# Optimization experiments

Hardware: AMD Instinct MI355X
Metric: run time of the kernel (lower is better)

Reference implementation:

```python
import jax, jax.numpy as jnp
import numpy as np

WS = 14            # window side (14x14 patches)
DIM = 768          # model dim (ViT-Base)
H = 12             # heads
HD = DIM // H      # head dim = 64
B = 128            # batch
N = WS * WS + 1    # 197 tokens (patches + CLS)
NRD = (2 * WS - 1) ** 2 + 3  # num_relative_distance = 732


def _rel_index():
    # Faithful replication of the torch buffer construction.
    coords = np.stack(np.meshgrid(np.arange(WS), np.arange(WS), indexing='ij'))  # [2,WS,WS]
    flat = coords.reshape(2, -1)                                   # [2, WS*WS]
    rel = flat[:, :, None] - flat[:, None, :]                      # [2, P, P]
    rel = rel.transpose(1, 2, 0).astype(np.int64)                  # [P, P, 2]
    rel[:, :, 0] += WS - 1
    rel[:, :, 1] += WS - 1
    rel[:, :, 0] *= 2 * WS - 1
    idx = np.zeros((N, N), dtype=np.int64)
    idx[1:, 1:] = rel.sum(-1)
    idx[0, :] = NRD - 3
    idx[:, 0] = NRD - 2
    idx[0, 0] = NRD - 1
    return jnp.asarray(idx, dtype=jnp.int32)


def setup_inputs() -> dict:
    key = jax.random.key(0)
    ks = jax.random.split(key, 5)
    return {
        'x': jax.random.normal(ks[0], (B, N, DIM), dtype=jnp.float32),
        'qkv_w': jax.random.normal(ks[1], (3 * DIM, DIM), dtype=jnp.float32) * 0.02,
        'q_bias': jnp.zeros((DIM,), jnp.float32),
        'v_bias': jnp.zeros((DIM,), jnp.float32),
        'rpb_table': jax.random.normal(ks[2], (NRD, H), dtype=jnp.float32) * 0.02,
        'proj_w': jax.random.normal(ks[3], (DIM, DIM), dtype=jnp.float32) * 0.02,
        'proj_b': jnp.zeros((DIM,), jnp.float32),
        'rel_idx': _rel_index(),
    }


def reference(x, qkv_w, q_bias, v_bias, rpb_table, proj_w, proj_b, rel_idx):
    Bv, Nv, C = x.shape
    scale = HD ** -0.5
    # qkv_bias = cat(q_bias, zeros, v_bias); eval mode so dropout is identity
    bias = jnp.concatenate([q_bias, jnp.zeros_like(v_bias), v_bias])
    qkv = x @ qkv_w.T + bias                                   # [B,N,3*DIM]
    qkv = qkv.reshape(Bv, Nv, 3, H, HD).transpose(2, 0, 3, 1, 4)
    q, k, v = qkv[0] * scale, qkv[1], qkv[2]                   # [B,H,N,HD]
    attn = jnp.einsum('bhqd,bhkd->bhqk', q, k)                 # [B,H,N,N]
    rpb = rpb_table[rel_idx]                                   # gather -> [N,N,H]
    attn = attn + rpb.transpose(2, 0, 1)[None]                 # + [1,H,N,N]
    attn = jax.nn.softmax(attn, axis=-1)
    out = jnp.einsum('bhqk,bhkd->bhqd', attn, v)               # [B,H,N,HD]
    out = out.transpose(0, 2, 1, 3).reshape(Bv, Nv, H * HD)
    return out @ proj_w.T + proj_b
```

## Files before the change

### kernel.cpp

```cpp
#include <hip/hip_runtime.h>
#include <hip/hip_bf16.h>
#include <cstdint>

#define BATCH 128
#define NTOK  197
#define NHEAD 12

typedef __attribute__((ext_vector_type(8))) __bf16 bf16x8;
typedef __attribute__((ext_vector_type(4))) float f32x4;
typedef __attribute__((ext_vector_type(4))) unsigned short ushort4v;

#define KSTR 72

__device__ __forceinline__ unsigned short f2bf(float f) {
    union { float f; unsigned int u; } v; v.f = f;
    unsigned int r = (v.u + 0x7FFFu + ((v.u >> 16) & 1u)) >> 16;
    return (unsigned short)r;
}

__device__ __forceinline__ void async_cp16(const void* gsrc, void* lds_dst) {
    __builtin_amdgcn_global_load_lds(
        (const __attribute__((address_space(1))) unsigned int*)((uintptr_t)gsrc),
        (__attribute__((address_space(3))) unsigned int*)((uintptr_t)lds_dst),
        16, 0, 0);
}

__global__ void bias_tiles(const float* __restrict__ rpb,
                           const int* __restrict__ rel_idx,
                           float* __restrict__ BT) {
    int idx = blockIdx.x * 256 + threadIdx.x;
    int r    = idx & 3;
    int j    = (idx >> 2) & 3;
    int l16  = (idx >> 4) & 15;
    int quad = (idx >> 8) & 3;
    int kt   = (idx >> 10) & 3;
    int qt   = (idx >> 12) & 15;
    int h    = idx >> 16;
    int qn = qt * 16 + quad * 4 + r; if (qn > 196) qn = 196;
    int kn = kt * 64 + j * 16 + l16;
    float v = 0.f;
    if (kn < NTOK) v = rpb[rel_idx[qn * NTOK + kn] * NHEAD + h];
    BT[idx] = v;
}

__global__ __launch_bounds__(256) void cvt_bf16(const float4* __restrict__ src,
                                                ushort4v* __restrict__ dst, int n4) {
    int i = blockIdx.x * 256 + threadIdx.x;
    if (i >= n4) return;
    float4 f = src[i];
    ushort4v o;
    o.x = f2bf(f.x); o.y = f2bf(f.y); o.z = f2bf(f.z); o.w = f2bf(f.w);
    dst[i] = o;
}

template <int EPI>
__global__ __launch_bounds__(512, 2) void gemm_mfma(
    const unsigned short* __restrict__ A,
    const unsigned short* __restrict__ W,
    const float* __restrict__ bias1, const float* __restrict__ bias2,
    unsigned short* __restrict__ oq, unsigned short* __restrict__ ok,
    unsigned short* __restrict__ ov, float* __restrict__ outf,
    int Mc) {
    __shared__ unsigned short lds[65536];

    const int t    = threadIdx.x;
    const int lane = t & 63;
    const int wave = t >> 6;
    const int wm   = wave >> 2;
    const int wn   = wave & 3;
    const int quad = lane >> 4;
    const int l16  = lane & 15;
    const int m0   = blockIdx.y * 256;
    const int n0   = blockIdx.x * 256;

    const int srow = wave * 8 + (lane >> 3);
    const int scol = (((lane & 7) ^ (lane >> 3)) << 3);
    const unsigned short* Asrc[4];
    const unsigned short* Wsrc[4];
#pragma unroll
    for (int l = 0; l < 4; l++) {
        int ra = m0 + l * 64 + srow; if (ra >= Mc) ra = Mc - 1;
        Asrc[l] = A + (size_t)ra * 768 + scol;
        Wsrc[l] = W + (size_t)(n0 + l * 64 + srow) * 768 + scol;
    }

    auto stage = [&](int c, int kt) {
        unsigned short* Ab = lds + c * 32768;
        unsigned short* Bb = Ab + 16384;
#pragma unroll
        for (int l = 0; l < 4; l++) {
            async_cp16(Asrc[l] + kt * 64, Ab + (l * 64 + wave * 8) * 64);
            async_cp16(Wsrc[l] + kt * 64, Bb + (l * 64 + wave * 8) * 64);
        }
    };

    const int arow0 = wm * 128 + l16;
    const int brow0 = wn * 64 + l16;
    const int csw0  = ((quad ^ (l16 & 7)) << 3);
    const int csw1  = (((4 + quad) ^ (l16 & 7)) << 3);

    f32x4 acc[8][4] = {};

    stage(0, 0);
#pragma unroll 1
    for (int kt = 0; kt < 12; kt++) {
        const int c = kt & 1;
        if (kt < 11) {
            stage(c ^ 1, kt + 1);
            asm volatile("s_waitcnt vmcnt(8)" ::: "memory");
        } else {
            asm volatile("s_waitcnt vmcnt(0)" ::: "memory");
        }
        __builtin_amdgcn_s_barrier();
        __builtin_amdgcn_sched_barrier(0);

        const unsigned short* Ab = lds + c * 32768;
        const unsigned short* Bb = Ab + 16384;

        bf16x8 bfr[4][2];
#pragma unroll
        for (int nf = 0; nf < 4; nf++) {
            bfr[nf][0] = *(const bf16x8*)(Bb + (brow0 + nf * 16) * 64 + csw0);
            bfr[nf][1] = *(const bf16x8*)(Bb + (brow0 + nf * 16) * 64 + csw1);
        }
#pragma unroll
        for (int p = 0; p < 4; p++) {
            bf16x8 af[2][2];
#pragma unroll
            for (int i = 0; i < 2; i++) {
                af[i][0] = *(const bf16x8*)(Ab + (arow0 + (p * 2 + i) * 16) * 64 + csw0);
                af[i][1] = *(const bf16x8*)(Ab + (arow0 + (p * 2 + i) * 16) * 64 + csw1);
            }
            __builtin_amdgcn_s_barrier();
            __builtin_amdgcn_sched_barrier(0);
            __builtin_amdgcn_s_setprio(1);
#pragma unroll
            for (int kk = 0; kk < 2; kk++)
#pragma unroll
                for (int i = 0; i < 2; i++)
#pragma unroll
                    for (int nf = 0; nf < 4; nf++)
                        acc[p * 2 + i][nf] = __builtin_amdgcn_mfma_f32_16x16x32_bf16(
                            af[i][kk], bfr[nf][kk], acc[p * 2 + i][nf], 0, 0, 0);
            __builtin_amdgcn_s_setprio(0);
            __builtin_amdgcn_sched_barrier(0);
            __builtin_amdgcn_s_barrier();
        }
    }

    if (EPI == 0) {
        const int part   = n0 / 768;
        const float scale = (part == 0) ? 0.125f : 1.f;
        unsigned short* dst = (part == 0) ? oq : (part == 1 ? ok : ov);
        const int nb = (n0 - part * 768) + wn * 64;
        const int h  = nb >> 6;
#pragma unroll
        for (int nf = 0; nf < 4; nf++) {
            const int d = nf * 16 + l16;
            const float bb = (part == 0) ? bias1[nb + nf * 16 + l16]
                           : (part == 2 ? bias2[nb + nf * 16 + l16] : 0.f);
#pragma unroll
            for (int mf = 0; mf < 8; mf++) {
                const int mb = m0 + wm * 128 + mf * 16 + quad * 4;
#pragma unroll
                for (int r = 0; r < 4; r++) {
                    const int m = mb + r;
                    if (m < Mc) {
                        const int bi  = m / NTOK;
                        const int tok = m - bi * NTOK;
                        dst[(((size_t)bi * NHEAD + h) * NTOK + tok) * 64 + d] =
                            f2bf((acc[mf][nf][r] + bb) * scale);
                    }
                }
            }
        }
    } else {
#pragma unroll
        for (int nf = 0; nf < 4; nf++) {
            const int col = n0 + wn * 64 + nf * 16 + l16;
            const float bb = bias1[col];
#pragma unroll
            for (int mf = 0; mf < 8; mf++) {
                const int mb = m0 + wm * 128 + mf * 16 + quad * 4;
#pragma unroll
                for (int r = 0; r < 4; r++) {
                    const int m = mb + r;
                    if (m < Mc) outf[(size_t)m * 768 + col] = acc[mf][nf][r] + bb;
                }
            }
        }
    }
}

__global__ __launch_bounds__(256, 2) void attn_mfma(
    const unsigned short* __restrict__ Q, const unsigned short* __restrict__ K,
    const unsigned short* __restrict__ V, const float* __restrict__ BT,
    unsigned short* __restrict__ AO) {
    __shared__ unsigned short Ks[64 * KSTR];
    __shared__ unsigned short Vt[64 * KSTR];
    __shared__ unsigned short Ps[4][64 * KSTR];

    const int t    = threadIdx.x;
    const int lane = t & 63;
    const int wave = t >> 6;
    const int quad = lane >> 4;
    const int l16  = lane & 15;
    const int bh   = blockIdx.x;
    const int b    = bh / NHEAD;
    const int h    = bh - b * NHEAD;

    const unsigned short* qb = Q + (size_t)bh * NTOK * 64;
    const unsigned short* kb = K + (size_t)bh * NTOK * 64;
    const unsigned short* vb = V + (size_t)bh * NTOK * 64;

    bf16x8 qf[4][2];
#pragma unroll
    for (int i = 0; i < 4; i++) {
        int tok = wave * 64 + i * 16 + l16; if (tok > 196) tok = 196;
#pragma unroll
        for (int ks = 0; ks < 2; ks++)
            qf[i][ks] = *(const bf16x8*)&qb[(size_t)tok * 64 + ks * 32 + quad * 8];
    }

    f32x4 O[4][4] = {};
    float lsum[4][4] = {};

    for (int kt = 0; kt < 4; kt++) {
        __syncthreads();
        {
            const int row = t >> 2, cg = t & 3;
            int gk = kt * 64 + row; if (gk > 196) gk = 196;
            const uint4* src = (const uint4*)&kb[(size_t)gk * 64 + cg * 16];
            *(uint4*)&Ks[row * KSTR + cg * 16]     = src[0];
            *(uint4*)&Ks[row * KSTR + cg * 16 + 8] = src[1];
        }
        {
            const int key = t & 63, dg = t >> 6;
            int gk = kt * 64 + key; if (gk > 196) gk = 196;
            union { uint4 v4[2]; unsigned short u[16]; } tmp;
            const uint4* src = (const uint4*)&vb[(size_t)gk * 64 + dg * 16];
            tmp.v4[0] = src[0]; tmp.v4[1] = src[1];
#pragma unroll
            for (int u = 0; u < 16; u++) Vt[(dg * 16 + u) * KSTR + key] = tmp.u[u];
        }
        __syncthreads();

        f32x4 acc[4][4];
#pragma unroll
        for (int i = 0; i < 4; i++) {
            const float4* bp = (const float4*)&BT[
                (((((size_t)h * 16 + (wave * 4 + i)) * 4 + kt) * 4 + quad) * 16 + l16) * 16];
#pragma unroll
            for (int j = 0; j < 4; j++) {
                float4 f = bp[j];
                acc[i][j] = (f32x4){f.x, f.y, f.z, f.w};
            }
        }

#pragma unroll
        for (int ks = 0; ks < 2; ks++) {
            bf16x8 kf[4];
#pragma unroll
            for (int j = 0; j < 4; j++)
                kf[j] = *(const bf16x8*)&Ks[(j * 16 + l16) * KSTR + ks * 32 + quad * 8];
#pragma unroll
            for (int i = 0; i < 4; i++)
#pragma unroll
                for (int j = 0; j < 4; j++)
                    acc[i][j] = __builtin_amdgcn_mfma_f32_16x16x32_bf16(
                        qf[i][ks], kf[j], acc[i][j], 0, 0, 0);
        }

#pragma unroll
        for (int j = 0; j < 4; j++) {
            const int kn = kt * 64 + j * 16 + l16;
            const bool kval = (kn < NTOK);
#pragma unroll
            for (int i = 0; i < 4; i++)
#pragma unroll
                for (int r = 0; r < 4; r++) {
                    float p = kval ? __expf(fminf(acc[i][j][r], 30.f)) : 0.f;
                    lsum[i][r] += p;
                    Ps[wave][(i * 16 + quad * 4 + r) * KSTR + j * 16 + l16] = f2bf(p);
                }
        }

#pragma unroll
        for (int ks = 0; ks < 2; ks++) {
            bf16x8 vf[4], pf[4];
#pragma unroll
            for (int jd = 0; jd < 4; jd++)
                vf[jd] = *(const bf16x8*)&Vt[(jd * 16 + l16) * KSTR + ks * 32 + quad * 8];
#pragma unroll
            for (int i = 0; i < 4; i++)
                pf[i] = *(const bf16x8*)&Ps[wave][(i * 16 + l16) * KSTR + ks * 32 + quad * 8];
#pragma unroll
            for (int i = 0; i < 4; i++)
#pragma unroll
                for (int jd = 0; jd < 4; jd++)
                    O[i][jd] = __builtin_amdgcn_mfma_f32_16x16x32_bf16(
                        pf[i], vf[jd], O[i][jd], 0, 0, 0);
        }
    }

#pragma unroll
    for (int i = 0; i < 4; i++)
#pragma unroll
        for (int r = 0; r < 4; r++) {
            float l = lsum[i][r];
            l += __shfl_xor(l, 1); l += __shfl_xor(l, 2);
            l += __shfl_xor(l, 4); l += __shfl_xor(l, 8);
            lsum[i][r] = 1.f / l;
        }
#pragma unroll
    for (int i = 0; i < 4; i++) {
        const int tb = wave * 64 + i * 16 + quad * 4;
#pragma unroll
        for (int r = 0; r < 4; r++) {
            const int tok = tb + r;
            if (tok < NTOK) {
                const float rl = lsum[i][r];
#pragma unroll
                for (int jd = 0; jd < 4; jd++)
                    AO[((size_t)b * NTOK + tok) * 768 + h * 64 + jd * 16 + l16] =
                        f2bf(O[i][jd][r] * rl);
            }
        }
    }
}

extern "C" void kernel_launch(void* const* d_in, const int* in_sizes, int n_in,
                              void* d_out, int out_size, void* d_ws, size_t ws_size,
                              hipStream_t stream) {
    const float* x      = (const float*)d_in[0];
    const float* qkv_w  = (const float*)d_in[1];
    const float* q_bias = (const float*)d_in[2];
    const float* v_bias = (const float*)d_in[3];
    const float* rpb    = (const float*)d_in[4];
    const float* proj_w = (const float*)d_in[5];
    const float* proj_b = (const float*)d_in[6];
    const int*   rel_idx = (const int*)d_in[7];
    float* out = (float*)d_out;

    const size_t EB   = 151296;
    const size_t NBT  = 786432;
    const size_t NX   = (size_t)BATCH * NTOK * 768;
    const size_t NWQ  = (size_t)2304 * 768;
    const size_t NWP  = (size_t)768 * 768;

    const size_t fixed_bytes = NBT * 4 + (NX + NWQ + NWP) * 2;
    int Bc = BATCH;
    while (Bc > 1 && fixed_bytes + 8ull * Bc * EB > ws_size) Bc >>= 1;
    if (fixed_bytes + 8ull * Bc * EB > ws_size) return;
    const int nc = BATCH / Bc;
    const int Mc = Bc * NTOK;
    const int Gy = (Mc + 255) / 256;

    float* BT             = (float*)d_ws;
    unsigned short* xbf   = (unsigned short*)(BT + NBT);
    unsigned short* wqkv  = xbf + NX;
    unsigned short* wproj = wqkv + NWQ;
    unsigned short* q     = wproj + NWP;
    unsigned short* k     = q + (size_t)Bc * EB;
    unsigned short* v     = k + (size_t)Bc * EB;
    unsigned short* aobf  = v + (size_t)Bc * EB;

    bias_tiles<<<(int)(NBT / 256), 256, 0, stream>>>(rpb, rel_idx, BT);
    cvt_bf16<<<(int)((NX / 4 + 255) / 256), 256, 0, stream>>>(
        (const float4*)x, (ushort4v*)xbf, (int)(NX / 4));
    cvt_bf16<<<(int)((NWQ / 4 + 255) / 256), 256, 0, stream>>>(
        (const float4*)qkv_w, (ushort4v*)wqkv, (int)(NWQ / 4));
    cvt_bf16<<<(int)((NWP / 4 + 255) / 256), 256, 0, stream>>>(
        (const float4*)proj_w, (ushort4v*)wproj, (int)(NWP / 4));

    for (int c = 0; c < nc; c++) {
        gemm_mfma<0><<<dim3(2304 / 256, Gy), 512, 0, stream>>>(
            xbf + (size_t)c * Mc * 768, wqkv, q_bias, v_bias, q, k, v, nullptr, Mc);
        attn_mfma<<<Bc * NHEAD, 256, 0, stream>>>(q, k, v, BT, aobf);
        gemm_mfma<1><<<dim3(768 / 256, Gy), 512, 0, stream>>>(
            aobf, wproj, proj_b, nullptr, nullptr, nullptr, nullptr,
            out + (size_t)c * Mc * 768, Mc);
    }
}
```

Measured before the change: 501.4 us.

## Remap workgroups per XCD and interleave half-tile prefetch with MFMA phases

Workgroup IDs are remapped so consecutive tiles land on the same XCD, aiming for better L2 reuse of A/W tiles. The global-to-LDS prefetch of the next K-tile is split into quarter stages issued inside the first two MFMA phases instead of all at once before compute. Per-phase trailing barriers are replaced by one waitcnt plus barrier per k-iteration. This targets load/compute overlap and barrier overhead, at the risk of LDS hazards if ordering is wrong.

```diff
diff --git a/kernel.cpp b/kernel.cpp
--- a/kernel.cpp
+++ b/kernel.cpp
@@ -70,68 +70,72 @@
     const int wn   = wave & 3;
     const int quad = lane >> 4;
     const int l16  = lane & 15;
-    const int m0   = blockIdx.y * 256;
-    const int n0   = blockIdx.x * 256;
+
+    const int gx  = gridDim.x;
+    const int nwg = gx * gridDim.y;
+    const int orig = blockIdx.y * gx + blockIdx.x;
+    const int q8 = nwg >> 3, r8 = nwg & 7;
+    const int xcd = orig & 7, rest = orig >> 3;
+    const int wg = (xcd < r8 ? xcd * (q8 + 1) : r8 * (q8 + 1) + (xcd - r8) * q8) + rest;
+    const int m0 = (wg / gx) * 256;
+    const int n0 = (wg % gx) * 256;
 
     const int srow = wave * 8 + (lane >> 3);
     const int scol = (((lane & 7) ^ (lane >> 3)) << 3);
-    const unsigned short* Asrc[4];
-    const unsigned short* Wsrc[4];
-#pragma unroll
-    for (int l = 0; l < 4; l++) {
-        int ra = m0 + l * 64 + srow; if (ra >= Mc) ra = Mc - 1;
-        Asrc[l] = A + (size_t)ra * 768 + scol;
-        Wsrc[l] = W + (size_t)(n0 + l * 64 + srow) * 768 + scol;
-    }
-
-    auto stage = [&](int c, int kt) {
-        unsigned short* Ab = lds + c * 32768;
-        unsigned short* Bb = Ab + 16384;
-#pragma unroll
-        for (int l = 0; l < 4; l++) {
-            async_cp16(Asrc[l] + kt * 64, Ab + (l * 64 + wave * 8) * 64);
-            async_cp16(Wsrc[l] + kt * 64, Bb + (l * 64 + wave * 8) * 64);
-        }
+    const unsigned short* gsrc[4][2];
+#pragma unroll
+    for (int hh = 0; hh < 2; hh++)
+#pragma unroll
+        for (int i = 0; i < 2; i++) {
+            int ra = m0 + hh * 128 + i * 64 + srow; if (ra >= Mc) ra = Mc - 1;
+            gsrc[hh][i]     = A + (size_t)ra * 768 + scol;
+            gsrc[2 + hh][i] = W + (size_t)(n0 + hh * 128 + i * 64 + srow) * 768 + scol;
+        }
+
+    auto stageHalf = [&](int b, int kt, int ht) {
+        unsigned short* dst = lds + b * 32768 + ht * 8192;
+        async_cp16(gsrc[ht][0] + kt * 64, dst + (wave * 8) * 64);
+        async_cp16(gsrc[ht][1] + kt * 64, dst + (64 + wave * 8) * 64);
     };
 
-    const int arow0 = wm * 128 + l16;
-    const int brow0 = wn * 64 + l16;
-    const int csw0  = ((quad ^ (l16 & 7)) << 3);
-    const int csw1  = (((4 + quad) ^ (l16 & 7)) << 3);
+    const int csw0 = ((quad ^ (l16 & 7)) << 3);
+    const int csw1 = (((4 + quad) ^ (l16 & 7)) << 3);
+    const int brow = (wn & 1) * 64 + l16;
 
     f32x4 acc[8][4] = {};
 
-    stage(0, 0);
-#pragma unroll 1
+#pragma unroll
+    for (int ht = 0; ht < 4; ht++) stageHalf(0, 0, ht);
+    asm volatile("s_waitcnt vmcnt(0)" ::: "memory");
+    __builtin_amdgcn_s_barrier();
+
+#pragma unroll 2
     for (int kt = 0; kt < 12; kt++) {
-        const int c = kt & 1;
-        if (kt < 11) {
-            stage(c ^ 1, kt + 1);
-            asm volatile("s_waitcnt vmcnt(8)" ::: "memory");
-        } else {
-            asm volatile("s_waitcnt vmcnt(0)" ::: "memory");
-        }
-        __builtin_amdgcn_s_barrier();
-        __builtin_amdgcn_sched_barrier(0);
-
-        const unsigned short* Ab = lds + c * 32768;
-        const unsigned short* Bb = Ab + 16384;
-
+        const int b = kt & 1;
+        const unsigned short* Ah = lds + b * 32768 + wm * 8192;
+        const unsigned short* Bh = lds + b * 32768 + 16384 + (wn >> 1) * 8192;
         bf16x8 bfr[4][2];
-#pragma unroll
-        for (int nf = 0; nf < 4; nf++) {
-            bfr[nf][0] = *(const bf16x8*)(Bb + (brow0 + nf * 16) * 64 + csw0);
-            bfr[nf][1] = *(const bf16x8*)(Bb + (brow0 + nf * 16) * 64 + csw1);
-        }
 #pragma unroll
         for (int p = 0; p < 4; p++) {
             bf16x8 af[2][2];
 #pragma unroll
             for (int i = 0; i < 2; i++) {
-                af[i][0] = *(const bf16x8*)(Ab + (arow0 + (p * 2 + i) * 16) * 64 + csw0);
-                af[i][1] = *(const bf16x8*)(Ab + (arow0 + (p * 2 + i) * 16) * 64 + csw1);
+                const int r = (p * 2 + i) * 16 + l16;
+                af[i][0] = *(const bf16x8*)(Ah + r * 64 + csw0);
+                af[i][1] = *(const bf16x8*)(Ah + r * 64 + csw1);
+            }
+            if (p == 0) {
+#pragma unroll
+                for (int nf = 0; nf < 4; nf++) {
+                    bfr[nf][0] = *(const bf16x8*)(Bh + (brow + nf * 16) * 64 + csw0);
+                    bfr[nf][1] = *(const bf16x8*)(Bh + (brow + nf * 16) * 64 + csw1);
+                }
+                if (kt < 11) { stageHalf(b ^ 1, kt + 1, 2); stageHalf(b ^ 1, kt + 1, 3); }
+            } else if (p == 1) {
+                if (kt < 11) { stageHalf(b ^ 1, kt + 1, 0); stageHalf(b ^ 1, kt + 1, 1); }
             }
             __builtin_amdgcn_s_barrier();
+            asm volatile("s_waitcnt lgkmcnt(0)" ::: "memory");
             __builtin_amdgcn_sched_barrier(0);
             __builtin_amdgcn_s_setprio(1);
 #pragma unroll
@@ -143,9 +147,9 @@
                         acc[p * 2 + i][nf] = __builtin_amdgcn_mfma_f32_16x16x32_bf16(
                             af[i][kk], bfr[nf][kk], acc[p * 2 + i][nf], 0, 0, 0);
             __builtin_amdgcn_s_setprio(0);
-            __builtin_amdgcn_sched_barrier(0);
-            __builtin_amdgcn_s_barrier();
-        }
+        }
+        asm volatile("s_waitcnt vmcnt(0)" ::: "memory");
+        __builtin_amdgcn_s_barrier();
     }
 
     if (EPI == 0) {
```

Result: faster. 477.5 us (-4.8%).
